# Kernel optimization log

Measured on AMD Instinct MI355X. Metric: run time of the kernel, lower is better.

Reference implementation:

```python
import jax, jax.numpy as jnp
import numpy as np

B, D_IN, D_HID, D_OUT = 1024, 4096, 4096, 2048
SPARSITY = 50
K_PR = int(SPARSITY * 1.5)        # sparsity * sparsity_boost = 75
K_SHIFT = SPARSITY + 1            # int(sparsity + 1) = 51
SUM_NORM = 1.0
GAIN = 2.0
EPS = 1e-13


def topk_mask(y, k):
    """1.0 at the top-k entries of each row (dim=1), else 0.0 (= build_topk_mask)."""
    _, idx = jax.lax.top_k(y, k)                      # [B, k]
    rows = jnp.arange(y.shape[0])[:, None]
    return jnp.zeros_like(y).at[rows, idx].set(1.0)


def setup_inputs() -> dict:
    key = jax.random.key(0)
    k0, k1, k2, k3 = jax.random.split(key, 4)
    inputs = jax.random.uniform(k0, (B, D_IN), dtype=jnp.float32)
    targets = jax.random.uniform(k1, (B, D_OUT), dtype=jnp.float32)  # BCE targets in [0,1]
    s1 = float(1.0 / np.sqrt(D_IN))
    s2 = float(1.0 / np.sqrt(D_HID))
    w_enc = jax.random.uniform(k2, (D_IN, D_HID), jnp.float32, -s1, s1)
    b_enc = jnp.zeros((D_HID,), jnp.float32)
    w_dec = jax.random.uniform(k3, (D_HID, D_OUT), jnp.float32, -s2, s2)
    b_dec = jnp.zeros((D_OUT,), jnp.float32)
    return {"inputs": inputs, "targets": targets, "w_enc": w_enc, "b_enc": b_enc,
            "w_dec": w_dec, "b_dec": b_dec}


def reference(inputs, targets, w_enc, b_enc, w_dec, b_dec):
    # SimpleAutoencoder forward: encoder Linear + nonlinearity, decoder Linear -> logits
    hidden = jax.nn.leaky_relu(inputs @ w_enc + b_enc)          # [B, D_HID]
    logits = hidden @ w_dec + b_dec                             # [B, D_OUT]

    # F.binary_cross_entropy_with_logits, mean reduction (numerically stable)
    loss = jnp.mean(jnp.maximum(logits, 0.0) - logits * targets
                    + jnp.log1p(jnp.exp(-jnp.abs(logits))))

    # post-hoc chain (detached in torch; forward math identical)
    y = jax.nn.sigmoid(logits)
    y = jnp.clip(y, 0.0, 1.0)
    # sparsen
    y = y * topk_mask(y, K_PR)
    # sum_norm > 0
    y_sum = jnp.sum(y, axis=1, keepdims=True)
    y = y * (1.0 / y_sum + EPS) * SUM_NORM
    # softmax (torch F.softmax default dim=1 for 2D)
    y = jax.nn.softmax(y, axis=1)
    # gain
    y = y * GAIN
    pr_out = y

    # shift_range: unit -> [-1, 1]
    z_cue_in = pr_out * 2.0 - 1.0

    # shift_bits: get_pc_topk_shift(pr_out, sparsity)
    cue_mask = topk_mask(pr_out, K_SHIFT)
    y_inv_masked_max = jnp.max((1.0 - pr_out) * cue_mask, axis=1)   # [B]
    y_masked_min = 1.0 - y_inv_masked_max
    cue_tanh_masked_min = y_masked_min * 2.0 - 1.0
    shift = (0.0 - cue_tanh_masked_min)[:, None]                    # [B, 1]
    z_cue = z_cue_in + shift

    return (loss, pr_out, z_cue_in, z_cue)
```

## Files before the change

kernel.cpp:

```cpp
#include <hip/hip_runtime.h>
#include <hip/hip_bf16.h>


typedef unsigned short u16;
typedef unsigned int u32;
typedef unsigned long long u64;
typedef __attribute__((ext_vector_type(4))) float f32x4;
typedef __attribute__((ext_vector_type(8))) short s16x8;

#define GAS __attribute__((address_space(1)))
#define LAS __attribute__((address_space(3)))

__device__ __forceinline__ u16 f2bf(float x) {
  u32 u = __float_as_uint(x);
  u32 r = (u + 0x7FFFu + ((u >> 16) & 1u)) >> 16;
  return (u16)r;
}

__device__ __forceinline__ void gld_lds16(const u16* g, u16* l) {
  __builtin_amdgcn_global_load_lds((const GAS void*)g, (LAS void*)l, 16, 0, 0);
}


__device__ __forceinline__ void tcast_body(const float* __restrict__ in,
                                           u16* __restrict__ out, int R, int C,
                                           int bx, int by, int tid) {
  __shared__ float tile[32][33];
  const int cb = bx * 32, rb = by * 32;
  const int tx = tid & 31, ty = tid >> 5;
#pragma unroll
  for (int i = 0; i < 4; i++)
    tile[ty + i * 8][tx] = in[(size_t)(rb + ty + i * 8) * C + cb + tx];
  __syncthreads();
#pragma unroll
  for (int i = 0; i < 4; i++)
    out[(size_t)(cb + ty + i * 8) * R + rb + tx] = f2bf(tile[tx][ty + i * 8]);
}

__global__ __launch_bounds__(256) void prep_kernel(
    const float* __restrict__ inputs, const float* __restrict__ w_enc,
    const float* __restrict__ w_dec, u16* __restrict__ A16,
    u16* __restrict__ W1T, u16* __restrict__ W2T) {
  const int bid = blockIdx.x, tid = threadIdx.x;
  if (bid < 4096) {
    const int i = bid * 256 + tid;
    float4 v = ((const float4*)inputs)[i];
    uint2 p;
    p.x = (u32)f2bf(v.x) | ((u32)f2bf(v.y) << 16);
    p.y = (u32)f2bf(v.z) | ((u32)f2bf(v.w) << 16);
    ((uint2*)A16)[i] = p;
  } else if (bid < 20480) {
    const int idx = bid - 4096;
    tcast_body(w_enc, W1T, 4096, 4096, idx & 127, idx >> 7, tid);
  } else {
    const int idx = bid - 20480;
    tcast_body(w_dec, W2T, 4096, 2048, idx & 63, idx >> 6, tid);
  }
}


template <int ACT>
__global__ __launch_bounds__(256, 2) void gemm2ph_kernel(
    const u16* __restrict__ A, const u16* __restrict__ BT,
    const float* __restrict__ bias, void* __restrict__ out,
    int M, int N, int K, int klen) {
  constexpr int BM = 128, BN = 128, BK = 64;
  constexpr int MF = 4, NF = 4;
  constexpr int BUF = BM * BK + BN * BK;
  __shared__ __align__(16) u16 smem[2 * BUF];

  const int tid = threadIdx.x;
  const int wid = tid >> 6, lane = tid & 63;
  const int wm = wid >> 1, wn = wid & 1;
  const int n0 = blockIdx.x * BN, m0 = blockIdx.y * BM;
  const int kbase = blockIdx.z * klen;

  f32x4 acc[MF][NF];
#pragma unroll
  for (int f = 0; f < MF; f++)
#pragma unroll
    for (int j = 0; j < NF; j++) acc[f][j] = (f32x4)0.f;

  const u16* Ag = A + (size_t)(m0 + (lane >> 3)) * K + kbase + (lane & 7) * 8;
  const u16* Bg = BT + (size_t)(n0 + (lane >> 3)) * K + kbase + (lane & 7) * 8;
  const int fr = lane & 15, fg = lane >> 4;
  const int NT = klen / BK;

  auto stage = [&](int b, int koff) {
    u16* Al = smem + b * BUF;
    u16* Bl = Al + BM * BK;
#pragma unroll
    for (int t2 = 0; t2 < 4; t2++) {
      const int i = wid * 4 + t2;
      gld_lds16(Ag + (size_t)i * 8 * K + koff, Al + i * 512);
      gld_lds16(Bg + (size_t)i * 8 * K + koff, Bl + i * 512);
    }
  };

  stage(0, 0);
  __syncthreads();
  int cur = 0;
  for (int t = 0; t < NT; t++) {
    if (t + 1 < NT) stage(cur ^ 1, (t + 1) * BK);

    const u16* Ab = smem + cur * BUF;
    const u16* Bb = Ab + BM * BK;
    s16x8 af[MF][2], bf[NF][2];
#pragma unroll
    for (int f = 0; f < MF; f++)
#pragma unroll
      for (int kk = 0; kk < 2; kk++)
        af[f][kk] = *(const s16x8*)&Ab[(wm * 64 + f * 16 + fr) * BK + kk * 32 + fg * 8];
#pragma unroll
    for (int j = 0; j < NF; j++)
#pragma unroll
      for (int kk = 0; kk < 2; kk++)
        bf[j][kk] = *(const s16x8*)&Bb[(wn * 64 + j * 16 + fr) * BK + kk * 32 + fg * 8];
#pragma unroll
    for (int kk = 0; kk < 2; kk++)
#pragma unroll
      for (int f = 0; f < MF; f++)
#pragma unroll
        for (int j = 0; j < NF; j++)
          acc[f][j] = __builtin_amdgcn_mfma_f32_16x16x32_bf16(
              af[f][kk], bf[j][kk], acc[f][j], 0, 0, 0);

    __syncthreads();
    cur ^= 1;
  }

#pragma unroll
  for (int j = 0; j < NF; j++) {
    const int col = n0 + wn * 64 + j * 16 + fr;
    const float bv = ACT ? bias[col] : 0.f;
#pragma unroll
    for (int f = 0; f < MF; f++) {
#pragma unroll
      for (int q = 0; q < 4; q++) {
        const int row = m0 + wm * 64 + f * 16 + fg * 4 + q;
        if (ACT) {
          float v = acc[f][j][q] + bv;
          v = (v > 0.f) ? v : 0.01f * v;
          ((u16*)out)[(size_t)row * N + col] = f2bf(v);
        } else {
          float* o = (float*)out + (size_t)blockIdx.z * M * N;
          o[(size_t)row * N + col] = acc[f][j][q];
        }
      }
    }
  }
}


__device__ __forceinline__ float wred_sum(float v) {
#pragma unroll
  for (int o = 32; o; o >>= 1) v += __shfl_xor(v, o, 64);
  return v;
}
__device__ __forceinline__ float wred_max(float v) {
#pragma unroll
  for (int o = 32; o; o >>= 1) v = fmaxf(v, __shfl_xor(v, o, 64));
  return v;
}
__device__ __forceinline__ u32 wred_sumu(u32 v) {
#pragma unroll
  for (int o = 32; o; o >>= 1) v += (u32)__shfl_xor((int)v, o, 64);
  return v;
}


__global__ __launch_bounds__(256, 1) void epilogue_wave_kernel(
    const float* __restrict__ p0, const float* __restrict__ p1,
    const float* __restrict__ p2, const float* __restrict__ p3,
    const float* __restrict__ b_dec, const float* __restrict__ targets,
    float* __restrict__ out, float* __restrict__ lossp) {
  const int tid = threadIdx.x;
  const int widx = tid >> 6, lane = tid & 63;
  const int r = blockIdx.x * 4 + widx;
  const size_t rb = (size_t)r * 2048;

  u32 u[32];
  float bce = 0.f, ymax = 0.f;
#pragma unroll
  for (int g = 0; g < 8; g++) {
    const size_t o = rb + g * 256 + lane * 4;
    float4 a = *(const float4*)(p0 + o);
    float4 b = *(const float4*)(p1 + o);
    float4 d = *(const float4*)(p2 + o);
    float4 e = *(const float4*)(p3 + o);
    float4 c4 = *(const float4*)(b_dec + g * 256 + lane * 4);
    float4 t4 = *(const float4*)(targets + o);
    float lv[4] = {a.x + b.x + d.x + e.x + c4.x, a.y + b.y + d.y + e.y + c4.y,
                   a.z + b.z + d.z + e.z + c4.z, a.w + b.w + d.w + e.w + c4.w};
    float tv[4] = {t4.x, t4.y, t4.z, t4.w};
#pragma unroll
    for (int j = 0; j < 4; j++) {
      float li = lv[j];
      bce += fmaxf(li, 0.f) - li * tv[j] + log1pf(expf(-fabsf(li)));
      float yi = 1.f / (1.f + expf(-li));
      u[g * 4 + j] = __float_as_uint(yi);
      ymax = fmaxf(ymax, yi);
    }
  }
  bce = wred_sum(bce);
  if (lane == 0) lossp[r] = bce;
  ymax = wred_max(ymax);

  u32 T75 = 0, T51 = 0;
  for (int b = 29; b >= 0; b--) {
    const u32 c75 = T75 | (1u << b), c51 = T51 | (1u << b);
    u32 cnt = 0;
#pragma unroll
    for (int i = 0; i < 32; i++) {
      cnt += (u[i] >= c75) ? 1u : 0u;
      cnt += (u[i] >= c51) ? 0x10000u : 0u;
    }
    cnt = wred_sumu(cnt);
    if ((cnt & 0xFFFFu) >= 75u) T75 = c75;
    if ((cnt >> 16) >= 51u) T51 = c51;
  }

  u32 cc = 0; float sgt = 0.f;
#pragma unroll
  for (int i = 0; i < 32; i++) {
    if (u[i] > T75)       { cc += 1u; sgt += __uint_as_float(u[i]); }
    else if (u[i] == T75) { cc += 0x10000u; }
  }
  cc = wred_sumu(cc);
  sgt = wred_sum(sgt);
  const u32 G = cc & 0xFFFFu, E = cc >> 16;
  const u32 need = 75u - G;
  const float t75f = __uint_as_float(T75);
  const float ysum = sgt + (float)need * t75f;

  u32 selmask = 0;
#pragma unroll
  for (int i = 0; i < 32; i++)
    if (u[i] >= T75) selmask |= (1u << i);
  if (need != E) {
    const u64 ltm = ((u64)1 << lane) - 1ull;
    u32 cum = 0;
#pragma unroll
    for (int g = 0; g < 8; g++) {
      u64 bm[4];
      u32 below = 0, grp = 0;
#pragma unroll
      for (int j = 0; j < 4; j++) {
        bm[j] = __ballot(u[g * 4 + j] == T75);
        below += (u32)__popcll(bm[j] & ltm);
        grp += (u32)__popcll(bm[j]);
      }
      u32 same = 0;
#pragma unroll
      for (int j = 0; j < 4; j++) {
        const int r2 = g * 4 + j;
        if (u[r2] == T75) {
          if (cum + below + same >= need) selmask &= ~(1u << r2);
          same++;
        }
      }
      cum += grp;
    }
  }

  const float c = 1.f / ysum + 1e-13f;
  const float Mv = c * ymax;
  float zs = 0.f;
#pragma unroll
  for (int i = 0; i < 32; i++) {
    float yi = __uint_as_float(u[i]);
    float v = ((selmask >> i) & 1u) ? c * yi : 0.f;
    float e = expf(v - Mv);
    zs += e;
    u[i] = __float_as_uint(e);
  }
  const float Z = wred_sum(zs);
  const float gZ = 2.f / Z;
  const float shift = 1.f - 2.f * (expf(c * __uint_as_float(T51) - Mv) * gZ);

  float* pr_o = out + 1;
  float* zi_o = out + 1 + 2097152;
  float* zc_o = out + 1 + 4194304;
#pragma unroll
  for (int g = 0; g < 8; g++) {
    float4 pr4, zi4, zc4;
    float e0 = __uint_as_float(u[g * 4 + 0]) * gZ;
    float e1 = __uint_as_float(u[g * 4 + 1]) * gZ;
    float e2 = __uint_as_float(u[g * 4 + 2]) * gZ;
    float e3 = __uint_as_float(u[g * 4 + 3]) * gZ;
    pr4 = make_float4(e0, e1, e2, e3);
    zi4 = make_float4(2.f * e0 - 1.f, 2.f * e1 - 1.f, 2.f * e2 - 1.f,
                      2.f * e3 - 1.f);
    zc4 = make_float4(zi4.x + shift, zi4.y + shift, zi4.z + shift,
                      zi4.w + shift);
    const size_t o = rb + g * 256 + lane * 4;
    *(float4*)(pr_o + o) = pr4;
    *(float4*)(zi_o + o) = zi4;
    *(float4*)(zc_o + o) = zc4;
  }
}

__global__ void loss_reduce_kernel(const float* __restrict__ lp,
                                   float* __restrict__ out) {
  const int tid = threadIdx.x;
  float s = 0.f;
  for (int i = tid; i < 1024; i += 256) s += lp[i];
  __shared__ float sf[4];
  float v = s;
#pragma unroll
  for (int o = 32; o; o >>= 1) v += __shfl_down(v, o, 64);
  if ((tid & 63) == 0) sf[tid >> 6] = v;
  __syncthreads();
  if (tid == 0) out[0] = (sf[0] + sf[1] + sf[2] + sf[3]) * (1.f / (1024.f * 2048.f));
}


extern "C" void kernel_launch(void* const* d_in, const int* in_sizes, int n_in,
                              void* d_out, int out_size, void* d_ws, size_t ws_size,
                              hipStream_t stream) {
  (void)in_sizes; (void)n_in; (void)out_size; (void)ws_size;
  const float* inputs  = (const float*)d_in[0];
  const float* targets = (const float*)d_in[1];
  const float* w_enc   = (const float*)d_in[2];
  const float* b_enc   = (const float*)d_in[3];
  const float* w_dec   = (const float*)d_in[4];
  const float* b_dec   = (const float*)d_in[5];
  float* out = (float*)d_out;

  char* ws = (char*)d_ws;
  u16* A16 = (u16*)ws;
  u16* W1T = (u16*)(ws + (8u << 20));
  u16* W2T = (u16*)(ws + (40u << 20));
  u16* H16 = (u16*)(ws + (56u << 20));
  float* lgts  = (float*)(ws + (8u << 20));
  float* lossp = (float*)ws;

  prep_kernel<<<28672, 256, 0, stream>>>(inputs, w_enc, w_dec, A16, W1T, W2T);

  gemm2ph_kernel<1><<<dim3(32, 8), 256, 0, stream>>>(
      A16, W1T, b_enc, (void*)H16, 1024, 4096, 4096, 4096);
  gemm2ph_kernel<0><<<dim3(16, 8, 4), 256, 0, stream>>>(
      H16, W2T, nullptr, (void*)lgts, 1024, 2048, 4096, 1024);

  const float* q0 = lgts;
  const float* q1 = lgts + (size_t)2 * 1024 * 1024;
  const float* q2 = lgts + (size_t)4 * 1024 * 1024;
  const float* q3 = lgts + (size_t)6 * 1024 * 1024;
  epilogue_wave_kernel<<<256, 256, 0, stream>>>(q0, q1, q2, q3, b_dec,
                                                targets, out, lossp);
  loss_reduce_kernel<<<1, 256, 0, stream>>>(lossp, out);
}
```

Baseline: 288.5 us.

## Swizzle GEMM LDS layout, unroll double buffer, widen transpose-cast stores

The GEMM now applies an XOR swizzle to the 16-byte chunk index when loading global data into LDS and when reading MFMA fragments. This is meant to avoid LDS bank conflicts on the fragment reads. The double-buffer loop is manually unrolled by two with fixed buffer pointers, which removes the runtime buffer-index arithmetic. The weight transpose-cast tiles now cover 64 rows and write packed pairs of bf16 as 32-bit stores, halving the prep grid and widening its global writes.

```diff
diff --git a/kernel.cpp b/kernel.cpp
--- a/kernel.cpp
+++ b/kernel.cpp
@@ -25,16 +25,20 @@
 __device__ __forceinline__ void tcast_body(const float* __restrict__ in,
                                            u16* __restrict__ out, int R, int C,
                                            int bx, int by, int tid) {
-  __shared__ float tile[32][33];
-  const int cb = bx * 32, rb = by * 32;
+  __shared__ float tile[64][33];
+  const int cb = bx * 32, rb = by * 64;
   const int tx = tid & 31, ty = tid >> 5;
 #pragma unroll
-  for (int i = 0; i < 4; i++)
+  for (int i = 0; i < 8; i++)
     tile[ty + i * 8][tx] = in[(size_t)(rb + ty + i * 8) * C + cb + tx];
   __syncthreads();
 #pragma unroll
-  for (int i = 0; i < 4; i++)
-    out[(size_t)(cb + ty + i * 8) * R + rb + tx] = f2bf(tile[tx][ty + i * 8]);
+  for (int i = 0; i < 4; i++) {
+    const int oc = ty + i * 8;
+    float v0 = tile[2 * tx][oc], v1 = tile[2 * tx + 1][oc];
+    u32 p = (u32)f2bf(v0) | ((u32)f2bf(v1) << 16);
+    *(u32*)(out + (size_t)(cb + oc) * R + rb + 2 * tx) = p;
+  }
 }
 
 __global__ __launch_bounds__(256) void prep_kernel(
@@ -49,11 +53,11 @@
     p.x = (u32)f2bf(v.x) | ((u32)f2bf(v.y) << 16);
     p.y = (u32)f2bf(v.z) | ((u32)f2bf(v.w) << 16);
     ((uint2*)A16)[i] = p;
-  } else if (bid < 20480) {
+  } else if (bid < 12288) {
     const int idx = bid - 4096;
     tcast_body(w_enc, W1T, 4096, 4096, idx & 127, idx >> 7, tid);
   } else {
-    const int idx = bid - 20480;
+    const int idx = bid - 12288;
     tcast_body(w_dec, W2T, 4096, 2048, idx & 63, idx >> 6, tid);
   }
 }
@@ -75,20 +79,24 @@
   const int n0 = blockIdx.x * BN, m0 = blockIdx.y * BM;
   const int kbase = blockIdx.z * klen;
 
+  u16* const A0 = smem;
+  u16* const B0 = smem + BM * BK;
+  u16* const A1 = smem + BUF;
+  u16* const B1 = smem + BUF + BM * BK;
+
   f32x4 acc[MF][NF];
 #pragma unroll
   for (int f = 0; f < MF; f++)
 #pragma unroll
     for (int j = 0; j < NF; j++) acc[f][j] = (f32x4)0.f;
 
-  const u16* Ag = A + (size_t)(m0 + (lane >> 3)) * K + kbase + (lane & 7) * 8;
-  const u16* Bg = BT + (size_t)(n0 + (lane >> 3)) * K + kbase + (lane & 7) * 8;
+  const int sg = (lane & 7) ^ ((lane >> 3) & 7);
+  const u16* Ag = A + (size_t)(m0 + (lane >> 3)) * K + kbase + sg * 8;
+  const u16* Bg = BT + (size_t)(n0 + (lane >> 3)) * K + kbase + sg * 8;
   const int fr = lane & 15, fg = lane >> 4;
   const int NT = klen / BK;
 
-  auto stage = [&](int b, int koff) {
-    u16* Al = smem + b * BUF;
-    u16* Bl = Al + BM * BK;
+  auto stage = [&](u16* __restrict__ Al, u16* __restrict__ Bl, int koff) {
 #pragma unroll
     for (int t2 = 0; t2 < 4; t2++) {
       const int i = wid * 4 + t2;
@@ -97,25 +105,21 @@
     }
   };
 
-  stage(0, 0);
-  __syncthreads();
-  int cur = 0;
-  for (int t = 0; t < NT; t++) {
-    if (t + 1 < NT) stage(cur ^ 1, (t + 1) * BK);
-
-    const u16* Ab = smem + cur * BUF;
-    const u16* Bb = Ab + BM * BK;
+  const int swz = fr & 7;
+  auto compute = [&](const u16* __restrict__ Ab, const u16* __restrict__ Bb) {
     s16x8 af[MF][2], bf[NF][2];
 #pragma unroll
     for (int f = 0; f < MF; f++)
 #pragma unroll
       for (int kk = 0; kk < 2; kk++)
-        af[f][kk] = *(const s16x8*)&Ab[(wm * 64 + f * 16 + fr) * BK + kk * 32 + fg * 8];
+        af[f][kk] = *(const s16x8*)
+            &Ab[(wm * 64 + f * 16 + fr) * BK + (((kk * 4 + fg) ^ swz) * 8)];
 #pragma unroll
     for (int j = 0; j < NF; j++)
 #pragma unroll
       for (int kk = 0; kk < 2; kk++)
-        bf[j][kk] = *(const s16x8*)&Bb[(wn * 64 + j * 16 + fr) * BK + kk * 32 + fg * 8];
+        bf[j][kk] = *(const s16x8*)
+            &Bb[(wn * 64 + j * 16 + fr) * BK + (((kk * 4 + fg) ^ swz) * 8)];
 #pragma unroll
     for (int kk = 0; kk < 2; kk++)
 #pragma unroll
@@ -124,9 +128,17 @@
         for (int j = 0; j < NF; j++)
           acc[f][j] = __builtin_amdgcn_mfma_f32_16x16x32_bf16(
               af[f][kk], bf[j][kk], acc[f][j], 0, 0, 0);
-
+  };
+
+  stage(A0, B0, 0);
+  __syncthreads();
+  for (int t = 0; t < NT; t += 2) {
+    if (t + 1 < NT) stage(A1, B1, (t + 1) * BK);
+    compute(A0, B0);
     __syncthreads();
-    cur ^= 1;
+    if (t + 2 < NT) stage(A0, B0, (t + 2) * BK);
+    compute(A1, B1);
+    __syncthreads();
   }
 
 #pragma unroll
@@ -335,7 +347,7 @@
   float* lgts  = (float*)(ws + (8u << 20));
   float* lossp = (float*)ws;
 
-  prep_kernel<<<28672, 256, 0, stream>>>(inputs, w_enc, w_dec, A16, W1T, W2T);
+  prep_kernel<<<16384, 256, 0, stream>>>(inputs, w_enc, w_dec, A16, W1T, W2T);
 
   gemm2ph_kernel<1><<<dim3(32, 8), 256, 0, stream>>>(
       A16, W1T, b_enc, (void*)H16, 1024, 4096, 4096, 4096);
```

Result: faster. 281.5 us (-2.4%).
